# Kernel tuning notes

Hardware: AMD Instinct MI355X
Metric: run time of the kernel (lower is better)

Reference implementation:

```python
import jax, jax.numpy as jnp
import numpy as np

B, L1, L2, D = 16, 512, 512, 512
H, INNER = 8, 1024
HD = INNER // H  # 128

def _glorot(key, shape):
    fan_in, fan_out = shape[-2], shape[-1]
    lim = jnp.sqrt(6.0 / (fan_in + fan_out))
    return jax.random.uniform(key, shape, jnp.float32, -lim, lim)

def setup_inputs() -> dict:
    key = jax.random.key(0)
    ks = jax.random.split(key, 8)
    return {
        "primary": jax.random.normal(ks[0], (B, L1, D), jnp.float32),
        "secondary": jax.random.normal(ks[1], (B, L2, D), jnp.float32),
        "primary_mask": jnp.ones((B, L1), jnp.float32),
        "secondary_mask": jnp.ones((B, L2), jnp.float32),
        "W_aff": _glorot(ks[2], (H, D, D)),          # per-head bilinear affinity weights
        "W_p": _glorot(ks[3], (D, INNER)),            # linear_primary (no bias)
        "W_s": _glorot(ks[4], (D, INNER)),            # linear_secondary (no bias)
        "W_fp": _glorot(ks[5], (D + HD, D)),          # ffn_primary
        "b_fp": jnp.zeros((D,), jnp.float32),
        "W_fs": _glorot(ks[6], (D + HD, D)),          # ffn_secondary
        "b_fs": jnp.zeros((D,), jnp.float32),
    }

def reference(primary, secondary, primary_mask, secondary_mask,
              W_aff, W_p, W_s, W_fp, b_fp, W_fs, b_fs):
    b, l1, d = primary.shape
    l2 = secondary.shape[1]
    h = W_aff.shape[0]
    hd = W_p.shape[1] // h
    # affinity mask: (B, 1, L1, L2)
    mask = (primary_mask[:, :, None] * secondary_mask[:, None, :])[:, None, :, :]
    # multi-head bilinear affinity: tanh(P Wk S^T) -> (B, H, L1, L2)
    aff = jnp.tanh(jnp.einsum('bie,hef,bjf->bhij', primary, W_aff, secondary)) * mask
    # project + split heads -> (B, H, L, hd)
    pp = (primary @ W_p).reshape(b, l1, h, hd).transpose(0, 2, 1, 3)
    ps = (secondary @ W_s).reshape(b, l2, h, hd).transpose(0, 2, 1, 3)
    # weighted sums (ReLU activation)
    wp = jax.nn.relu(jnp.einsum('bhij,bhid->bhjd', aff, pp))  # (B, H, L2, hd)
    ws = jax.nn.relu(jnp.einsum('bhij,bhjd->bhid', aff, ps))  # (B, H, L1, hd)
    # GlobalMaxPool1D applied to (L, H, hd) per sample => max over heads
    pool_p = wp.max(axis=1)  # (B, L2, hd)
    pool_s = ws.max(axis=1)  # (B, L1, hd)
    out_p = jax.nn.relu(jnp.concatenate([primary, pool_s], -1) @ W_fp + b_fp)
    out_s = jax.nn.relu(jnp.concatenate([secondary, pool_p], -1) @ W_fs + b_fs)
    return out_p, out_s
```

## Files before the change

### kernel.cpp

```cpp
#include <hip/hip_runtime.h>
#include <hip/hip_bf16.h>

typedef short short8 __attribute__((ext_vector_type(8)));
typedef float f32x16 __attribute__((ext_vector_type(16)));
typedef float f32x4 __attribute__((ext_vector_type(4)));

#define BM 128
#define BN 128

typedef const __attribute__((address_space(1))) void gas_t;
typedef __attribute__((address_space(3))) void las_t;

__device__ __forceinline__ unsigned short f2bf(float f) {
  unsigned int u = __float_as_uint(f);
  u += 0x7FFFu + ((u >> 16) & 1u);
  return (unsigned short)(u >> 16);
}

__device__ __forceinline__ unsigned int pmaxu16(unsigned int a, unsigned int b) {
  unsigned int lo = ((a & 0xFFFFu) > (b & 0xFFFFu)) ? (a & 0xFFFFu) : (b & 0xFFFFu);
  unsigned int hi = ((a >> 16) > (b >> 16)) ? (a & 0xFFFF0000u) : (b & 0xFFFF0000u);
  return lo | hi;
}

__device__ __forceinline__ float fast_tanh(float x) {
  x = fminf(fmaxf(x, -10.f), 10.f);
  float t = __builtin_amdgcn_exp2f(x * 2.8853900817779268f);
  return 1.f - 2.f * __builtin_amdgcn_rcpf(t + 1.f);
}

struct GemmP {
  const unsigned short* A;
  const unsigned short* Bm;
  void* C;
  const float* A2f;
  const unsigned short* A_b;
  const unsigned short* Bm_b;
  void* C_b;
  const float* A2f_b;
  const float* mask_p;
  const float* mask_s;
  const float* bias;
  const float* bias_b;
  long long sAb, sAh, sBb, sBh, sCb, sCh;
  int lda, lda2, ldb, ldc, M, N, K, Hh, kSplit, zSplit, nbx, nby;
};

template <int TA, int EPI>
__device__ __forceinline__ void gemm_body(const GemmP& p, int bx, int by, int bz, char* smem_) {
  constexpr int PA = (TA == 0) ? 32 : 40;
  constexpr int HSA = (TA == 0) ? 4096 : 5120;
  unsigned short* As = (unsigned short*)smem_;
  unsigned short* Bs = (unsigned short*)(smem_ + 2 * HSA * 2);

  int z = bz;
  const unsigned short* Abase = p.A;
  const unsigned short* Bbase = p.Bm;
  void* Cvp = p.C;
  const float* A2f = p.A2f;
  const float* bias = p.bias;
  if (p.zSplit && z >= p.zSplit) {
    z -= p.zSplit;
    Abase = p.A_b; Bbase = p.Bm_b; Cvp = p.C_b; A2f = p.A2f_b; bias = p.bias_b;
  }
  const int zb = z / p.Hh, zh = z % p.Hh;
  const unsigned short* A = Abase + (size_t)zb * p.sAb + (size_t)zh * p.sAh;
  const unsigned short* B = Bbase + (size_t)zb * p.sBb + (size_t)zh * p.sBh;
  const int m0 = bx * BM, n0 = by * BN;
  const int tid = threadIdx.x;
  const int wid = tid >> 6, lane = tid & 63;
  const int wm = (wid >> 1) * 64, wn = (wid & 1) * 64;
  const int lrow = lane & 31;
  const int lk8 = (lane >> 5) * 8;

  f32x16 acc[2][2] = {};

  const int dm = tid >> 2, dkg = tid & 3;

  auto mfma_block = [&]() {
#pragma unroll
    for (int h = 0; h < 2; ++h)
#pragma unroll
      for (int kc = 0; kc < 2; ++kc) {
        short8 af[2], bfv[2];
#pragma unroll
        for (int mt = 0; mt < 2; ++mt)
          af[mt] = *(const short8*)&As[h * HSA + (wm + mt * 32 + lrow) * PA + kc * 16 + lk8];
#pragma unroll
        for (int nt = 0; nt < 2; ++nt)
          bfv[nt] = *(const short8*)&Bs[h * 4096 + (wn + nt * 32 + lrow) * 32 + kc * 16 + lk8];
#pragma unroll
        for (int mt = 0; mt < 2; ++mt)
#pragma unroll
          for (int nt = 0; nt < 2; ++nt)
            acc[mt][nt] = __builtin_amdgcn_mfma_f32_32x32x16_bf16(af[mt], bfv[nt], acc[mt][nt], 0, 0, 0);
      }
  };
  auto stage_b = [&](int k0) {
#pragma unroll
    for (int h = 0; h < 2; ++h)
#pragma unroll
      for (int q = 0; q < 2; ++q) {
        const unsigned short* src = B + (size_t)(n0 + q * 64 + dm) * p.ldb + (k0 + h * 32 + dkg * 8);
        __builtin_amdgcn_global_load_lds((gas_t*)src,
                                         (las_t*)&Bs[h * 4096 + q * 2048 + wid * 512],
                                         16, 0, 0);
      }
  };

  const int nIter = p.K >> 6;
  const int nIter1 = p.kSplit ? (p.kSplit >> 6) : nIter;

  for (int it = 0; it < nIter1; ++it) {
    const int k0 = it << 6;
    if (TA == 0) {
#pragma unroll
      for (int h = 0; h < 2; ++h)
#pragma unroll
        for (int q = 0; q < 2; ++q) {
          const unsigned short* src = A + (size_t)(m0 + q * 64 + dm) * p.lda + (k0 + h * 32 + dkg * 8);
          __builtin_amdgcn_global_load_lds((gas_t*)src,
                                           (las_t*)&As[h * HSA + q * 2048 + wid * 512],
                                           16, 0, 0);
        }
    } else {
      const int kk = tid & 31, mg = (tid >> 5) << 4;
#pragma unroll
      for (int h = 0; h < 2; ++h) {
        const unsigned short* src = A + (size_t)(k0 + h * 32 + kk) * p.lda + (m0 + mg);
        uint4 v0 = *(const uint4*)src;
        uint4 v1 = *(const uint4*)(src + 8);
        unsigned short tmp[16];
        *(uint4*)&tmp[0] = v0;
        *(uint4*)&tmp[8] = v1;
#pragma unroll
        for (int j = 0; j < 16; ++j) As[h * HSA + (mg + j) * PA + kk] = tmp[j];
      }
    }
    stage_b(k0);
    __syncthreads();
    mfma_block();
    __syncthreads();
  }

  if (TA == 0 && p.kSplit) {
    const unsigned short* planes = (const unsigned short*)A2f;
    for (int it = nIter1; it < nIter; ++it) {
      const int k0 = it << 6;
#pragma unroll
      for (int h2 = 0; h2 < 2; ++h2) {
        const int ko = k0 + h2 * 32 - p.kSplit;
#pragma unroll
        for (int q = 0; q < 2; ++q) {
          const int row = m0 + q * 64 + dm;
          const unsigned int* s0 = (const unsigned int*)(planes
              + ((size_t)(((row >> 9) << 12) + (row & 511)) * 128 + ko + dkg * 8));
          uint4 mv = *(const uint4*)s0;
#pragma unroll
          for (int hh = 1; hh < 8; ++hh) {
            uint4 v = *(const uint4*)(s0 + (size_t)hh * 32768);
            mv.x = pmaxu16(mv.x, v.x);
            mv.y = pmaxu16(mv.y, v.y);
            mv.z = pmaxu16(mv.z, v.z);
            mv.w = pmaxu16(mv.w, v.w);
          }
          *(uint4*)&As[h2 * HSA + (q * 64 + dm) * 32 + dkg * 8] = mv;
        }
      }
      stage_b(k0);
      __syncthreads();
      mfma_block();
      __syncthreads();
    }
  }

  unsigned short* Cu = (unsigned short*)Cvp + (size_t)zb * p.sCb + (size_t)zh * p.sCh;
  float* Cf = (float*)Cvp + (size_t)zb * p.sCb + (size_t)zh * p.sCh;

  const int rbase = 4 * (lane >> 5);

  float mp[2][16], ms[2];
  if constexpr (EPI == 1) {
#pragma unroll
    for (int mt = 0; mt < 2; ++mt)
#pragma unroll
      for (int reg = 0; reg < 16; ++reg) {
        const int rl = (reg & 3) + 8 * (reg >> 2) + rbase;
        mp[mt][reg] = p.mask_p[(size_t)zb * p.M + (m0 + wm + mt * 32 + rl)];
      }
#pragma unroll
    for (int nt = 0; nt < 2; ++nt)
      ms[nt] = p.mask_s[(size_t)zb * p.N + (n0 + wn + nt * 32 + lrow)];
  }
  if constexpr (EPI == 3) {
#pragma unroll
    for (int nt = 0; nt < 2; ++nt)
      ms[nt] = bias[n0 + wn + nt * 32 + lrow];
  }

#pragma unroll
  for (int mt = 0; mt < 2; ++mt) {
#pragma unroll
    for (int nt = 0; nt < 2; ++nt) {
      f32x16 a = acc[mt][nt];
#pragma unroll
      for (int reg = 0; reg < 16; ++reg) {
        const int rl = (reg & 3) + 8 * (reg >> 2) + rbase;
        const int grow = m0 + wm + mt * 32 + rl;
        const int gcol = n0 + wn + nt * 32 + lrow;
        const size_t idx = (size_t)grow * p.ldc + gcol;
        const float v = a[reg];
        if constexpr (EPI == 0) {
          Cu[idx] = f2bf(v);
        } else if constexpr (EPI == 1) {
          Cu[idx] = f2bf(fast_tanh(v) * (mp[mt][reg] * ms[nt]));
        } else if constexpr (EPI == 3) {
          Cf[idx] = fmaxf(v + ms[nt], 0.f);
        } else {
          Cu[idx] = f2bf(fmaxf(v, 0.f));
        }
      }
    }
  }
}

template <int TA, int EPI>
__global__ __launch_bounds__(256) void gemm_k(GemmP p) {
  extern __shared__ char smem[];
  gemm_body<TA, EPI>(p, blockIdx.x, blockIdx.y, blockIdx.z, smem);
}

template <int EPI>
__device__ __forceinline__ void gemm11_body(const GemmP& p, int bx, int by, int bz, char* smem_) {
  int z = bz;
  const unsigned short* Abase = p.A;
  const unsigned short* Bbase = p.Bm;
  void* Cvp = p.C;
  if (p.zSplit && z >= p.zSplit) {
    z -= p.zSplit;
    Abase = p.A_b; Bbase = p.Bm_b; Cvp = p.C_b;
  }
  const int zb = z / p.Hh, zh = z % p.Hh;
  const unsigned short* A = Abase + (size_t)zb * p.sAb + (size_t)zh * p.sAh;
  const unsigned short* B = Bbase + (size_t)zb * p.sBb + (size_t)zh * p.sBh;
  const int m0 = bx * 256, n0 = by * 128;
  const int tid = threadIdx.x;
  const int wid = tid >> 6, lane = tid & 63;
  const int wm = wid >> 1, wn = wid & 1;
  const int lrow = lane & 15, lhi = lane >> 4;

  const int rr = tid >> 3;
  const int cs = ((tid & 7) * 8) ^ ((rr & 7) << 3);

  const int colx = (lhi * 16) ^ ((lrow & 7) << 4);
  const int offA = (wm * 128 + lrow) * 128 + colx;
  const int offB = 32768 + (wn * 64 + lrow) * 128 + colx;

  f32x4 acc[8][4] = {};

  const int nt = p.K >> 6;

  for (int t = 0; t < nt; ++t) {
    const int k0 = t << 6;
    const unsigned short* sa = A + (size_t)(m0 + rr) * p.lda + k0 + cs;
#pragma unroll
    for (int s = 0; s < 8; ++s)
      __builtin_amdgcn_global_load_lds((gas_t*)(sa + (size_t)(s * 32) * p.lda),
                                       (las_t*)(smem_ + s * 4096 + tid * 16), 16, 0, 0);
    const unsigned short* sb = B + (size_t)(n0 + rr) * p.ldb + k0 + cs;
#pragma unroll
    for (int s = 0; s < 4; ++s)
      __builtin_amdgcn_global_load_lds((gas_t*)(sb + (size_t)(s * 32) * p.ldb),
                                       (las_t*)(smem_ + 32768 + s * 4096 + tid * 16), 16, 0, 0);
    __syncthreads();

    short8 af[4], bv[4];
#pragma unroll
    for (int fn = 0; fn < 4; ++fn) bv[fn] = *(const short8*)(smem_ + offB + fn * 2048);
#pragma unroll
    for (int fm = 0; fm < 4; ++fm) af[fm] = *(const short8*)(smem_ + offA + fm * 2048);
    __builtin_amdgcn_s_setprio(1);
#pragma unroll
    for (int fm = 0; fm < 4; ++fm)
#pragma unroll
      for (int fn = 0; fn < 4; ++fn)
        acc[fm][fn] = __builtin_amdgcn_mfma_f32_16x16x32_bf16(af[fm], bv[fn], acc[fm][fn], 0, 0, 0);
    __builtin_amdgcn_s_setprio(0);

#pragma unroll
    for (int fm = 0; fm < 4; ++fm) af[fm] = *(const short8*)(smem_ + offA + (4 + fm) * 2048);
    __builtin_amdgcn_s_setprio(1);
#pragma unroll
    for (int fm = 0; fm < 4; ++fm)
#pragma unroll
      for (int fn = 0; fn < 4; ++fn)
        acc[4 + fm][fn] = __builtin_amdgcn_mfma_f32_16x16x32_bf16(af[fm], bv[fn], acc[4 + fm][fn], 0, 0, 0);
    __builtin_amdgcn_s_setprio(0);

#pragma unroll
    for (int fn = 0; fn < 4; ++fn) bv[fn] = *(const short8*)(smem_ + (offB ^ 64) + fn * 2048);
#pragma unroll
    for (int fm = 0; fm < 4; ++fm) af[fm] = *(const short8*)(smem_ + (offA ^ 64) + fm * 2048);
    __builtin_amdgcn_s_setprio(1);
#pragma unroll
    for (int fm = 0; fm < 4; ++fm)
#pragma unroll
      for (int fn = 0; fn < 4; ++fn)
        acc[fm][fn] = __builtin_amdgcn_mfma_f32_16x16x32_bf16(af[fm], bv[fn], acc[fm][fn], 0, 0, 0);
    __builtin_amdgcn_s_setprio(0);

#pragma unroll
    for (int fm = 0; fm < 4; ++fm) af[fm] = *(const short8*)(smem_ + (offA ^ 64) + (4 + fm) * 2048);
    __builtin_amdgcn_s_setprio(1);
#pragma unroll
    for (int fm = 0; fm < 4; ++fm)
#pragma unroll
      for (int fn = 0; fn < 4; ++fn)
        acc[4 + fm][fn] = __builtin_amdgcn_mfma_f32_16x16x32_bf16(af[fm], bv[fn], acc[4 + fm][fn], 0, 0, 0);
    __builtin_amdgcn_s_setprio(0);

    if (t + 1 < nt) __syncthreads();
  }

  unsigned short* Cu = (unsigned short*)Cvp + (size_t)zb * p.sCb + (size_t)zh * p.sCh;

  float ms[4];
  if constexpr (EPI == 1) {
#pragma unroll
    for (int fn = 0; fn < 4; ++fn)
      ms[fn] = p.mask_s[(size_t)zb * p.N + (n0 + wn * 64 + fn * 16 + lrow)];
  }

#pragma unroll
  for (int fm = 0; fm < 8; ++fm)
#pragma unroll
    for (int fn = 0; fn < 4; ++fn) {
      f32x4 a = acc[fm][fn];
      const int gcol = n0 + wn * 64 + fn * 16 + lrow;
#pragma unroll
      for (int reg = 0; reg < 4; ++reg) {
        const int grow = m0 + wm * 128 + fm * 16 + lhi * 4 + reg;
        const size_t idx = (size_t)grow * p.ldc + gcol;
        if constexpr (EPI == 0) {
          Cu[idx] = f2bf(a[reg]);
        } else if constexpr (EPI == 4) {
          Cu[idx] = f2bf(fmaxf(a[reg], 0.f));
        } else {
          const float mp = p.mask_p[(size_t)zb * p.M + grow];
          Cu[idx] = f2bf(fast_tanh(a[reg]) * (mp * ms[fn]));
        }
      }
    }
}

template <int EPI>
__global__ __launch_bounds__(256, 2) void gemm11_k(GemmP p) {
  extern __shared__ char smem[];
  gemm11_body<EPI>(p, blockIdx.x, blockIdx.y, blockIdx.z, smem);
}

template <int E1, int E2>
__global__ __launch_bounds__(256, 2) void gemm11_pair_k(GemmP a, GemmP b, int nA) {
  extern __shared__ char smem[];
  int bid = blockIdx.x;
  if (bid < nA) {
    const int per = a.nbx * a.nby;
    const int z = bid / per, r = bid % per;
    gemm11_body<E1>(a, r % a.nbx, r / a.nbx, z, smem);
  } else {
    bid -= nA;
    const int per = b.nbx * b.nby;
    const int z = bid / per, r = bid % per;
    gemm11_body<E2>(b, r % b.nbx, r / b.nbx, z, smem);
  }
}

template <int E1, int TA2, int E2>
__global__ __launch_bounds__(256, 2) void mix_pair_k(GemmP a, GemmP b, int nA) {
  extern __shared__ char smem[];
  int bid = blockIdx.x;
  if (bid < nA) {
    const int per = a.nbx * a.nby;
    const int z = bid / per, r = bid % per;
    gemm11_body<E1>(a, r % a.nbx, r / a.nbx, z, smem);
  } else {
    bid -= nA;
    const int per = b.nbx * b.nby;
    const int z = bid / per, r = bid % per;
    gemm_body<TA2, E2>(b, r % b.nbx, r / b.nbx, z, smem);
  }
}

__device__ __forceinline__ void trans_body(const float* src, unsigned short* dst,
                                           int R, int C, int bx, int by, float (*tile)[33]) {
  const int r0 = by * 32, c0 = bx * 32;
  const int tx = threadIdx.x & 31, ty = threadIdx.x >> 5;
#pragma unroll
  for (int j = 0; j < 4; ++j)
    tile[ty + j * 8][tx] = src[(size_t)(r0 + ty + j * 8) * C + (c0 + tx)];
  __syncthreads();
#pragma unroll
  for (int j = 0; j < 4; ++j)
    dst[(size_t)(c0 + ty + j * 8) * R + (r0 + tx)] = f2bf(tile[tx][ty + j * 8]);
}

__global__ __launch_bounds__(256) void prep_k(const float* P, const float* S,
                                              unsigned short* Pbf, unsigned short* Sbf,
                                              const float* W_aff, unsigned short* WaT,
                                              const float* W_p, unsigned short* WpT,
                                              const float* W_s, unsigned short* WsT,
                                              const float* W_fp, unsigned short* WfpT,
                                              const float* W_fs, unsigned short* WfsT) {
  __shared__ float tile[32][33];
  const int bid = blockIdx.x;
  if (bid < 8192) {
    const int n4 = 1048576;
    int i = bid * 256 + threadIdx.x;
    const float4* s = (const float4*)P;
    ushort4* d = (ushort4*)Pbf;
    if (i >= n4) { i -= n4; s = (const float4*)S; d = (ushort4*)Sbf; }
    float4 v = s[i];
    ushort4 o;
    o.x = f2bf(v.x); o.y = f2bf(v.y); o.z = f2bf(v.z); o.w = f2bf(v.w);
    d[i] = o;
  } else if (bid < 10240) {
    const int l = bid - 8192;
    const int z = l >> 8, r = l & 255;
    trans_body(W_aff + (size_t)z * 262144, WaT + (size_t)z * 262144, 512, 512,
               r & 15, r >> 4, tile);
  } else if (bid < 11264) {
    const int l = bid - 10240;
    const int z = l >> 9, r = l & 511;
    trans_body(z ? W_s : W_p, z ? WsT : WpT, 512, 1024, r & 31, r >> 5, tile);
  } else {
    const int l = bid - 11264;
    const int z = l / 320, r = l % 320;
    trans_body(z ? W_fs : W_fp, z ? WfsT : WfpT, 640, 512, r & 15, r >> 4, tile);
  }
}

extern "C" void kernel_launch(void* const* d_in, const int* in_sizes, int n_in,
                              void* d_out, int out_size, void* d_ws, size_t ws_size,
                              hipStream_t stream) {
  (void)in_sizes; (void)n_in; (void)out_size; (void)ws_size;
  const float* primary   = (const float*)d_in[0];
  const float* secondary = (const float*)d_in[1];
  const float* pmask     = (const float*)d_in[2];
  const float* smask     = (const float*)d_in[3];
  const float* W_aff     = (const float*)d_in[4];
  const float* W_p       = (const float*)d_in[5];
  const float* W_s       = (const float*)d_in[6];
  const float* W_fp      = (const float*)d_in[7];
  const float* b_fp      = (const float*)d_in[8];
  const float* W_fs      = (const float*)d_in[9];
  const float* b_fs      = (const float*)d_in[10];

  constexpr int Bb = 16, L = 512, Dd = 512, Hh = 8, HDd = 128, INNER = 1024, CAT = 640;
  constexpr int NT = Hh * Dd;
  constexpr long long LD = (long long)L * Dd;
  constexpr long long LL = (long long)L * L;

  static bool s_attr = [] {
    hipFuncSetAttribute(reinterpret_cast<const void*>(&gemm11_pair_k<0, 0>),
                        hipFuncAttributeMaxDynamicSharedMemorySize, 49152);
    hipFuncSetAttribute(reinterpret_cast<const void*>(&gemm11_k<1>),
                        hipFuncAttributeMaxDynamicSharedMemorySize, 49152);
    hipFuncSetAttribute(reinterpret_cast<const void*>(&mix_pair_k<4, 1, 4>),
                        hipFuncAttributeMaxDynamicSharedMemorySize, 49152);
    return true;
  }();
  (void)s_attr;

  char* base = (char*)d_ws;
  size_t off = 0;
  auto alloc = [&](size_t bytes) -> void* {
    void* r = base + off;
    off += (bytes + 255) & ~(size_t)255;
    return r;
  };

  unsigned short* Pbf   = (unsigned short*)alloc((size_t)Bb * L * Dd * 2);
  unsigned short* Sbf   = (unsigned short*)alloc((size_t)Bb * L * Dd * 2);
  unsigned short* WaT   = (unsigned short*)alloc((size_t)NT * Dd * 2);
  unsigned short* WpT   = (unsigned short*)alloc((size_t)INNER * Dd * 2);
  unsigned short* WsT   = (unsigned short*)alloc((size_t)INNER * Dd * 2);
  unsigned short* WfpT  = (unsigned short*)alloc((size_t)Dd * CAT * 2);
  unsigned short* WfsT  = (unsigned short*)alloc((size_t)Dd * CAT * 2);
  unsigned short* psT   = (unsigned short*)alloc((size_t)Bb * INNER * L * 2);
  unsigned short* ppT   = (unsigned short*)alloc((size_t)Bb * INNER * L * 2);
  unsigned short* Tbuf  = (unsigned short*)alloc((size_t)Bb * L * NT * 2);
  unsigned short* affb  = (unsigned short*)alloc((size_t)Bb * Hh * L * L * 2);

  unsigned short* wsBuf = Tbuf;
  unsigned short* wpBuf = Tbuf + (size_t)Bb * Hh * L * HDd;

  prep_k<<<dim3(11904), dim3(256), 0, stream>>>(primary, secondary, Pbf, Sbf,
                                                W_aff, WaT, W_p, WpT, W_s, WsT,
                                                W_fp, WfpT, W_fs, WfsT);

  {
    GemmP a{};
    a.A = Pbf; a.lda = Dd;
    a.Bm = WaT; a.ldb = Dd;
    a.C = Tbuf; a.ldc = NT;
    a.M = Bb * L; a.N = NT; a.K = Dd; a.Hh = 1; a.nbx = 32; a.nby = 32;

    GemmP b{};
    b.A = WsT; b.lda = Dd; b.sAb = 0;
    b.Bm = Sbf; b.ldb = Dd; b.sBb = LD;
    b.C = psT; b.ldc = L; b.sCb = (long long)INNER * L;
    b.A_b = WpT; b.Bm_b = Pbf; b.C_b = ppT;
    b.M = INNER; b.N = L; b.K = Dd; b.Hh = 1; b.zSplit = Bb; b.nbx = 4; b.nby = 4;

    gemm11_pair_k<0, 0><<<dim3(1024 + 512), dim3(256), 49152, stream>>>(a, b, 1024);
  }

  {
    GemmP g{};
    g.A = Tbuf; g.lda = NT; g.sAb = (long long)L * NT; g.sAh = Dd;
    g.Bm = Sbf; g.ldb = Dd; g.sBb = LD; g.sBh = 0;
    g.C = affb; g.ldc = L; g.sCb = (long long)Hh * LL; g.sCh = LL;
    g.mask_p = pmask; g.mask_s = smask;
    g.M = L; g.N = L; g.K = Dd; g.Hh = Hh;
    gemm11_k<1><<<dim3(2, 4, Bb * Hh), dim3(256), 49152, stream>>>(g);
  }

  {
    GemmP a{};
    a.A = affb; a.lda = L; a.sAb = (long long)Hh * LL; a.sAh = LL;
    a.Bm = psT; a.ldb = L; a.sBb = (long long)INNER * L; a.sBh = (long long)HDd * L;
    a.C = wsBuf; a.ldc = HDd; a.sCb = (long long)Hh * L * HDd; a.sCh = (long long)L * HDd;
    a.M = L; a.N = HDd; a.K = L; a.Hh = Hh; a.nbx = 2; a.nby = 1;

    GemmP b{};
    b.A = affb; b.lda = L; b.sAb = (long long)Hh * LL; b.sAh = LL;
    b.Bm = ppT; b.ldb = L; b.sBb = (long long)INNER * L; b.sBh = (long long)HDd * L;
    b.C = wpBuf; b.ldc = HDd; b.sCb = (long long)Hh * L * HDd; b.sCh = (long long)L * HDd;
    b.M = L; b.N = HDd; b.K = L; b.Hh = Hh; b.nbx = 4; b.nby = 1;

    mix_pair_k<4, 1, 4><<<dim3(256 + 512), dim3(256), 49152, stream>>>(a, b, 256);
  }

  {
    GemmP g{};
    g.A = Pbf; g.lda = Dd;
    g.A2f = (const float*)wsBuf; g.lda2 = HDd; g.kSplit = Dd;
    g.Bm = WfpT; g.ldb = CAT;
    g.C = d_out; g.ldc = Dd;
    g.bias = b_fp;
    g.A_b = Sbf; g.A2f_b = (const float*)wpBuf; g.Bm_b = WfsT;
    g.C_b = (float*)d_out + (size_t)Bb * L * Dd;
    g.bias_b = b_fs;
    g.M = Bb * L; g.N = Dd; g.K = CAT; g.Hh = 1; g.zSplit = 1;
    gemm_k<0, 3><<<dim3(64, 4, 2), dim3(256), 32768, stream>>>(g);
  }
}
```

Baseline: 305.0 us.

## Run GEMM tile with 8 waves of 64 rows each and split mixed pair launch

Changes the 256x128 bf16 MFMA GEMM body from 4 waves (each computing 128x64) to 8 waves of 512 threads (each computing 64x64), halving per-wave accumulators and loads per thread. Launch bounds change to 512 threads with 3 blocks per SM. The mixed paired launch for the two weighted-sum GEMMs is replaced by two separate launches. The aim is more latency hiding and lower register pressure, at the cost of more LDS traffic per FLOP and losing the concurrency of the paired launch.

```diff
diff --git a/kernel.cpp b/kernel.cpp
--- a/kernel.cpp
+++ b/kernel.cpp
@@ -231,7 +231,7 @@
 }
 
 template <int EPI>
-__device__ __forceinline__ void gemm11_body(const GemmP& p, int bx, int by, int bz, char* smem_) {
+__device__ __forceinline__ void gemm15_body(const GemmP& p, int bx, int by, int bz, char* smem_) {
   int z = bz;
   const unsigned short* Abase = p.A;
   const unsigned short* Bbase = p.Bm;
@@ -253,10 +253,10 @@
   const int cs = ((tid & 7) * 8) ^ ((rr & 7) << 3);
 
   const int colx = (lhi * 16) ^ ((lrow & 7) << 4);
-  const int offA = (wm * 128 + lrow) * 128 + colx;
+  const int offA = (wm * 64 + lrow) * 128 + colx;
   const int offB = 32768 + (wn * 64 + lrow) * 128 + colx;
 
-  f32x4 acc[8][4] = {};
+  f32x4 acc[4][4] = {};
 
   const int nt = p.K >> 6;
 
@@ -264,14 +264,14 @@
     const int k0 = t << 6;
     const unsigned short* sa = A + (size_t)(m0 + rr) * p.lda + k0 + cs;
 #pragma unroll
-    for (int s = 0; s < 8; ++s)
-      __builtin_amdgcn_global_load_lds((gas_t*)(sa + (size_t)(s * 32) * p.lda),
-                                       (las_t*)(smem_ + s * 4096 + tid * 16), 16, 0, 0);
+    for (int s = 0; s < 4; ++s)
+      __builtin_amdgcn_global_load_lds((gas_t*)(sa + (size_t)(s * 64) * p.lda),
+                                       (las_t*)(smem_ + s * 8192 + tid * 16), 16, 0, 0);
     const unsigned short* sb = B + (size_t)(n0 + rr) * p.ldb + k0 + cs;
 #pragma unroll
-    for (int s = 0; s < 4; ++s)
-      __builtin_amdgcn_global_load_lds((gas_t*)(sb + (size_t)(s * 32) * p.ldb),
-                                       (las_t*)(smem_ + 32768 + s * 4096 + tid * 16), 16, 0, 0);
+    for (int s = 0; s < 2; ++s)
+      __builtin_amdgcn_global_load_lds((gas_t*)(sb + (size_t)(s * 64) * p.ldb),
+                                       (las_t*)(smem_ + 32768 + s * 8192 + tid * 16), 16, 0, 0);
     __syncthreads();
 
     short8 af[4], bv[4];
@@ -288,16 +288,6 @@
     __builtin_amdgcn_s_setprio(0);
 
 #pragma unroll
-    for (int fm = 0; fm < 4; ++fm) af[fm] = *(const short8*)(smem_ + offA + (4 + fm) * 2048);
-    __builtin_amdgcn_s_setprio(1);
-#pragma unroll
-    for (int fm = 0; fm < 4; ++fm)
-#pragma unroll
-      for (int fn = 0; fn < 4; ++fn)
-        acc[4 + fm][fn] = __builtin_amdgcn_mfma_f32_16x16x32_bf16(af[fm], bv[fn], acc[4 + fm][fn], 0, 0, 0);
-    __builtin_amdgcn_s_setprio(0);
-
-#pragma unroll
     for (int fn = 0; fn < 4; ++fn) bv[fn] = *(const short8*)(smem_ + (offB ^ 64) + fn * 2048);
 #pragma unroll
     for (int fm = 0; fm < 4; ++fm) af[fm] = *(const short8*)(smem_ + (offA ^ 64) + fm * 2048);
@@ -309,16 +299,6 @@
         acc[fm][fn] = __builtin_amdgcn_mfma_f32_16x16x32_bf16(af[fm], bv[fn], acc[fm][fn], 0, 0, 0);
     __builtin_amdgcn_s_setprio(0);
 
-#pragma unroll
-    for (int fm = 0; fm < 4; ++fm) af[fm] = *(const short8*)(smem_ + (offA ^ 64) + (4 + fm) * 2048);
-    __builtin_amdgcn_s_setprio(1);
-#pragma unroll
-    for (int fm = 0; fm < 4; ++fm)
-#pragma unroll
-      for (int fn = 0; fn < 4; ++fn)
-        acc[4 + fm][fn] = __builtin_amdgcn_mfma_f32_16x16x32_bf16(af[fm], bv[fn], acc[4 + fm][fn], 0, 0, 0);
-    __builtin_amdgcn_s_setprio(0);
-
     if (t + 1 < nt) __syncthreads();
   }
 
@@ -332,14 +312,14 @@
   }
 
 #pragma unroll
-  for (int fm = 0; fm < 8; ++fm)
+  for (int fm = 0; fm < 4; ++fm)
 #pragma unroll
     for (int fn = 0; fn < 4; ++fn) {
       f32x4 a = acc[fm][fn];
       const int gcol = n0 + wn * 64 + fn * 16 + lrow;
 #pragma unroll
       for (int reg = 0; reg < 4; ++reg) {
-        const int grow = m0 + wm * 128 + fm * 16 + lhi * 4 + reg;
+        const int grow = m0 + wm * 64 + fm * 16 + lhi * 4 + reg;
         const size_t idx = (size_t)grow * p.ldc + gcol;
         if constexpr (EPI == 0) {
           Cu[idx] = f2bf(a[reg]);
@@ -354,40 +334,24 @@
 }
 
 template <int EPI>
-__global__ __launch_bounds__(256, 2) void gemm11_k(GemmP p) {
+__global__ __launch_bounds__(512, 3) void gemm15_k(GemmP p) {
   extern __shared__ char smem[];
-  gemm11_body<EPI>(p, blockIdx.x, blockIdx.y, blockIdx.z, smem);
+  gemm15_body<EPI>(p, blockIdx.x, blockIdx.y, blockIdx.z, smem);
 }
 
 template <int E1, int E2>
-__global__ __launch_bounds__(256, 2) void gemm11_pair_k(GemmP a, GemmP b, int nA) {
+__global__ __launch_bounds__(512, 3) void gemm15_pair_k(GemmP a, GemmP b, int nA) {
   extern __shared__ char smem[];
   int bid = blockIdx.x;
   if (bid < nA) {
     const int per = a.nbx * a.nby;
     const int z = bid / per, r = bid % per;
-    gemm11_body<E1>(a, r % a.nbx, r / a.nbx, z, smem);
+    gemm15_body<E1>(a, r % a.nbx, r / a.nbx, z, smem);
   } else {
     bid -= nA;
     const int per = b.nbx * b.nby;
     const int z = bid / per, r = bid % per;
-    gemm11_body<E2>(b, r % b.nbx, r / b.nbx, z, smem);
-  }
-}
-
-template <int E1, int TA2, int E2>
-__global__ __launch_bounds__(256, 2) void mix_pair_k(GemmP a, GemmP b, int nA) {
-  extern __shared__ char smem[];
-  int bid = blockIdx.x;
-  if (bid < nA) {
-    const int per = a.nbx * a.nby;
-    const int z = bid / per, r = bid % per;
-    gemm11_body<E1>(a, r % a.nbx, r / a.nbx, z, smem);
-  } else {
-    bid -= nA;
-    const int per = b.nbx * b.nby;
-    const int z = bid / per, r = bid % per;
-    gemm_body<TA2, E2>(b, r % b.nbx, r / b.nbx, z, smem);
+    gemm15_body<E2>(b, r % b.nbx, r / b.nbx, z, smem);
   }
 }
 
@@ -461,11 +425,11 @@
   constexpr long long LL = (long long)L * L;
 
   static bool s_attr = [] {
-    hipFuncSetAttribute(reinterpret_cast<const void*>(&gemm11_pair_k<0, 0>),
+    hipFuncSetAttribute(reinterpret_cast<const void*>(&gemm15_pair_k<0, 0>),
                         hipFuncAttributeMaxDynamicSharedMemorySize, 49152);
-    hipFuncSetAttribute(reinterpret_cast<const void*>(&gemm11_k<1>),
+    hipFuncSetAttribute(reinterpret_cast<const void*>(&gemm15_k<1>),
                         hipFuncAttributeMaxDynamicSharedMemorySize, 49152);
-    hipFuncSetAttribute(reinterpret_cast<const void*>(&mix_pair_k<4, 1, 4>),
+    hipFuncSetAttribute(reinterpret_cast<const void*>(&gemm15_k<4>),
                         hipFuncAttributeMaxDynamicSharedMemorySize, 49152);
     return true;
   }();
@@ -512,7 +476,7 @@
     b.A_b = WpT; b.Bm_b = Pbf; b.C_b = ppT;
     b.M = INNER; b.N = L; b.K = Dd; b.Hh = 1; b.zSplit = Bb; b.nbx = 4; b.nby = 4;
 
-    gemm11_pair_k<0, 0><<<dim3(1024 + 512), dim3(256), 49152, stream>>>(a, b, 1024);
+    gemm15_pair_k<0, 0><<<dim3(1024 + 512), dim3(512), 49152, stream>>>(a, b, 1024);
   }
 
   {
@@ -522,7 +486,7 @@
     g.C = affb; g.ldc = L; g.sCb = (long long)Hh * LL; g.sCh = LL;
     g.mask_p = pmask; g.mask_s = smask;
     g.M = L; g.N = L; g.K = Dd; g.Hh = Hh;
-    gemm11_k<1><<<dim3(2, 4, Bb * Hh), dim3(256), 49152, stream>>>(g);
+    gemm15_k<1><<<dim3(2, 4, Bb * Hh), dim3(512), 49152, stream>>>(g);
   }
 
   {
@@ -530,15 +494,17 @@
     a.A = affb; a.lda = L; a.sAb = (long long)Hh * LL; a.sAh = LL;
     a.Bm = psT; a.ldb = L; a.sBb = (long long)INNER * L; a.sBh = (long long)HDd * L;
     a.C = wsBuf; a.ldc = HDd; a.sCb = (long long)Hh * L * HDd; a.sCh = (long long)L * HDd;
-    a.M = L; a.N = HDd; a.K = L; a.Hh = Hh; a.nbx = 2; a.nby = 1;
-
+    a.M = L; a.N = HDd; a.K = L; a.Hh = Hh;
+    gemm15_k<4><<<dim3(2, 1, Bb * Hh), dim3(512), 49152, stream>>>(a);
+  }
+
+  {
     GemmP b{};
     b.A = affb; b.lda = L; b.sAb = (long long)Hh * LL; b.sAh = LL;
     b.Bm = ppT; b.ldb = L; b.sBb = (long long)INNER * L; b.sBh = (long long)HDd * L;
     b.C = wpBuf; b.ldc = HDd; b.sCb = (long long)Hh * L * HDd; b.sCh = (long long)L * HDd;
-    b.M = L; b.N = HDd; b.K = L; b.Hh = Hh; b.nbx = 4; b.nby = 1;
-
-    mix_pair_k<4, 1, 4><<<dim3(256 + 512), dim3(256), 49152, stream>>>(a, b, 256);
+    b.M = L; b.N = HDd; b.K = L; b.Hh = Hh;
+    gemm_k<1, 4><<<dim3(4, 1, Bb * Hh), dim3(256), 36864, stream>>>(b);
   }
 
   {
```

Result: no change. 299.4 us (-1.8%).
